# Kernel optimization log

Hardware: AMD Instinct MI355X
Metric: run time of the kernel (lower is better)

Reference implementation:

```python
import jax, jax.numpy as jnp
import numpy as np

B, V, S, D, H, G = 8, 321, 24, 256, 8, 10
K = -(-V // G)   # num_per_group = ceil(var_num/groups) = 33
DFF = 1024
DH = D // H

PARAM_SHAPES = dict(
    queries=(B, V, S, D),
    t_wq=(D, D), t_bq=(D,), t_wk=(D, D), t_bk=(D,), t_wv=(D, D), t_bv=(D,), t_wo=(D, D), t_bo=(D,),
    s_wq=(D, D), s_bq=(D,), s_wk=(D, D), s_bk=(D,), s_wv=(D, D), s_bv=(D,), s_wo=(D, D), s_bo=(D,),
    cluster=(S, G, D), conv_w=(G, K), conv_b=(G,),
    r_wq=(D, D), r_bq=(D,), r_wk=(D, D), r_bk=(D,), r_wv=(D, D), r_bv=(D,), r_wo=(D, D), r_bo=(D,),
    ln_t1_g=(D,), ln_t1_b=(D,), ln_t2_g=(D,), ln_t2_b=(D,),
    ln_d1_g=(D,), ln_d1_b=(D,), ln_d2_g=(D,), ln_d2_b=(D,),
    ft_w1=(D, DFF), ft_b1=(DFF,), ft_w2=(DFF, D), ft_b2=(D,),
    fd_w1=(D, DFF), fd_b1=(DFF,), fd_w2=(DFF, D), fd_b2=(D,),
)


def setup_inputs() -> dict:
    key = jax.random.key(0)
    out = {}
    for i, (n, sh) in enumerate(PARAM_SHAPES.items()):
        k = jax.random.fold_in(key, i)
        if n == 'queries':
            out[n] = jax.random.normal(k, sh, jnp.float32)
        elif n.startswith('ln') and n.endswith('_g'):
            out[n] = jnp.ones(sh, jnp.float32)
        elif '_b' in n:
            out[n] = jnp.zeros(sh, jnp.float32)
        else:
            out[n] = jax.random.normal(k, sh, jnp.float32) * 0.02
    return out


def _ln(x, g, b):
    m = x.mean(-1, keepdims=True)
    v = ((x - m) ** 2).mean(-1, keepdims=True)
    return (x - m) * jax.lax.rsqrt(v + 1e-5) * g + b


def _mha(xq, xkv, wq, bq, wk, bk, wv, bv, wo, bo):
    # FullAttention (no mask, eval -> no dropout)
    Bq, L, _ = xq.shape
    Skv = xkv.shape[1]
    q = (xq @ wq + bq).reshape(Bq, L, H, DH)
    k = (xkv @ wk + bk).reshape(Bq, Skv, H, DH)
    v = (xkv @ wv + bv).reshape(Bq, Skv, H, DH)
    A = jax.nn.softmax(jnp.einsum('blhe,bshe->bhls', q, k) / jnp.sqrt(jnp.float32(DH)), axis=-1)
    o = jnp.einsum('bhls,bshd->blhd', A, v).reshape(Bq, L, D)
    return o @ wo + bo


def _ffn(x, w1, b1, w2, b2):
    return jax.nn.gelu(x @ w1 + b1, approximate=False) @ w2 + b2


def _scx(x, wq, bq, wk, bk, wv, bv, wo, bo, cluster, conv_w, conv_b):
    # SCX_Block: top-k cluster routing + gather + grouped 1x1 conv + min-max/exp
    bs = x.shape[0]  # B*S
    xl = jnp.log(jax.nn.relu(x) + 1.0)
    cl = jnp.tile(cluster, (bs // S, 1, 1))                      # (bs, G, D)
    q = (cl @ wq + bq).reshape(bs, G, H, DH).transpose(0, 2, 1, 3)
    k = (xl @ wk + bk).reshape(bs, V, H, DH).transpose(0, 2, 1, 3)
    v = (xl @ wv + bv).reshape(bs, V, H, DH).transpose(0, 2, 1, 3)
    scores = jnp.einsum('bhge,bhve->bhgv', q, k) / jnp.sqrt(jnp.float32(DH))
    _, idx = jax.lax.top_k(scores, K)                            # (bs, H, G, K)
    gathered = jnp.take_along_axis(v[:, :, None, :, :], idx[..., None], axis=3)  # (bs,H,G,K,DH)
    # grouped Conv1d, kernel_size=1 -> per-group weighted sum over K channels
    mixed = jnp.einsum('bhgkd,gk->bhgd', gathered, conv_w) + conv_b[None, None, :, None]
    xmin = mixed.min(-1, keepdims=True)
    xmax = mixed.max(-1, keepdims=True)
    xn = jnp.exp((mixed - xmin) / jnp.maximum(xmax - xmin, 1e-6))
    feat = xn.transpose(0, 2, 1, 3).reshape(bs, G, D)            # 'bs h g d -> bs g (h d)'
    return feat @ wo + bo


def _forward(queries, t_wq, t_bq, t_wk, t_bk, t_wv, t_bv, t_wo, t_bo, s_wq, s_bq, s_wk, s_bk, s_wv, s_bv, s_wo, s_bo, cluster, conv_w, conv_b, r_wq, r_bq, r_wk, r_bk, r_wv, r_bv, r_wo, r_bo, ln_t1_g, ln_t1_b, ln_t2_g, ln_t2_b, ln_d1_g, ln_d1_b, ln_d2_g, ln_d2_b, ft_w1, ft_b1, ft_w2, ft_b2, fd_w1, fd_b1, fd_w2, fd_b2):
    # Route 1: temporal path over segments within each variable
    x = queries.reshape(B * V, S, D)
    x = x + _mha(x, x, t_wq, t_bq, t_wk, t_bk, t_wv, t_bv, t_wo, t_bo)
    x = _ln(x, ln_t1_g, ln_t1_b)
    x = _ln(x + _ffn(x, ft_w1, ft_b1, ft_w2, ft_b2), ln_t2_g, ln_t2_b)
    # Route 2: dimensional path across variables, per segment
    xd = x.reshape(B, V, S, D).transpose(0, 2, 1, 3).reshape(B * S, V, D)
    route = _scx(xd, s_wq, s_bq, s_wk, s_bk, s_wv, s_bv, s_wo, s_bo, cluster, conv_w, conv_b)
    xd = xd + _mha(xd, route, r_wq, r_bq, r_wk, r_bk, r_wv, r_bv, r_wo, r_bo)
    xd = _ln(xd, ln_d1_g, ln_d1_b)
    xd = _ln(xd + _ffn(xd, fd_w1, fd_b1, fd_w2, fd_b2), ln_d2_g, ln_d2_b)
    return xd.reshape(B, S, V, D).transpose(0, 2, 1, 3)


def reference(queries, t_wq, t_bq, t_wk, t_bk, t_wv, t_bv, t_wo, t_bo, s_wq, s_bq, s_wk, s_bk, s_wv, s_bv, s_wo, s_bo, cluster, conv_w, conv_b, r_wq, r_bq, r_wk, r_bk, r_wv, r_bv, r_wo, r_bo, ln_t1_g, ln_t1_b, ln_t2_g, ln_t2_b, ln_d1_g, ln_d1_b, ln_d2_g, ln_d2_b, ft_w1, ft_b1, ft_w2, ft_b2, fd_w1, fd_b1, fd_w2, fd_b2):
    return _forward(queries, t_wq, t_bq, t_wk, t_bk, t_wv, t_bv, t_wo, t_bo, s_wq, s_bq, s_wk, s_bk, s_wv, s_bv, s_wo, s_bo, cluster, conv_w, conv_b, r_wq, r_bq, r_wk, r_bk, r_wv, r_bv, r_wo, r_bo, ln_t1_g, ln_t1_b, ln_t2_g, ln_t2_b, ln_d1_g, ln_d1_b, ln_d2_g, ln_d2_b, ft_w1, ft_b1, ft_w2, ft_b2, fd_w1, fd_b1, fd_w2, fd_b2)
```

## Files before the change

### kernel.cpp

```cpp
#include <hip/hip_runtime.h>
#include <hip/hip_bf16.h>
#include <cmath>

typedef __hip_bfloat16 bf16;
typedef __attribute__((ext_vector_type(8))) short short8;
typedef __attribute__((ext_vector_type(4))) float f32x4;
typedef unsigned int u32;
typedef __attribute__((address_space(3))) u32 lds_u32;
typedef const __attribute__((address_space(1))) u32 glob_u32;

#define BB 8
#define VV 321
#define SS 24
#define DD 256
#define HH 8
#define GG 10
#define KTOP 33
#define DFFN 1024
#define BV (BB*VV)
#define BSEG (BB*SS)
#define NROWS (BV*SS)
#define NE ((size_t)NROWS*DD)
#define SCALE 0.17677669529663687f
#define A2CH 4

enum { GF_GELU=1, GF_LOGRELU=2, GF_ABF16=4, GF_RBF16=8, GF_CBF16=16 };
enum { MF_GELU=1, MF_RF32=8, MF_CF32=16, MF_SPLIT=32, MF_SWZ=64 };

__device__ __forceinline__ float bf2f(bf16 x){ return __bfloat162float(x); }
__device__ __forceinline__ unsigned short f2bfbits(float f){
  bf16 h = __float2bfloat16(f);
  return *(unsigned short*)&h;
}
__device__ __forceinline__ float bfbits2f(unsigned int u){
  bf16 h; *(unsigned short*)&h = (unsigned short)u; return __bfloat162float(h);
}
__device__ __forceinline__ void ld4bf(const bf16* p, float* f){
  uint2 u = *(const uint2*)p;
  f[0]=bfbits2f(u.x&0xffff); f[1]=bfbits2f(u.x>>16);
  f[2]=bfbits2f(u.y&0xffff); f[3]=bfbits2f(u.y>>16);
}
__device__ __forceinline__ void st4bf(bf16* p, const float* f){
  uint2 u;
  u.x = (unsigned)f2bfbits(f[0]) | ((unsigned)f2bfbits(f[1])<<16);
  u.y = (unsigned)f2bfbits(f[2]) | ((unsigned)f2bfbits(f[3])<<16);
  *(uint2*)p = u;
}
__device__ __forceinline__ void gl_lds16(const void* g, void* l){
  __builtin_amdgcn_global_load_lds((glob_u32*)g, (lds_u32*)l, 16, 0, 0);
}

struct WPrep {
  const float* src[12];
  int K[12], N[12], dstoff[12], tileoff[13];
};

__global__ __launch_bounds__(256) void prep_w_k(WPrep p, bf16* __restrict__ pool)
{
  __shared__ float t[32][33];
  int b = blockIdx.x;
  int m = 0;
  while (b >= p.tileoff[m+1]) ++m;
  int tt = b - p.tileoff[m];
  int K = p.K[m], N = p.N[m];
  int nc = N >> 5;
  int tr = tt / nc, tc = tt % nc;
  const float* src = p.src[m];
  int tid = threadIdx.x;
  int r = tid >> 3, c = (tid & 7) * 4;
  float4 v = *(const float4*)&src[(size_t)(tr*32 + r)*N + tc*32 + c];
  t[r][c+0]=v.x; t[r][c+1]=v.y; t[r][c+2]=v.z; t[r][c+3]=v.w;
  __syncthreads();
  bf16* dst = pool + p.dstoff[m];
  size_t base = (size_t)(tc*32 + r)*K + tr*32 + c;
  #pragma unroll
  for (int i=0;i<4;++i) dst[base+i] = __float2bfloat16(t[c+i][r]);
}

__global__ __launch_bounds__(256) void f2b_k(const float* __restrict__ X, bf16* __restrict__ Y, size_t n)
{
  size_t i = ((size_t)blockIdx.x*256 + threadIdx.x)*8;
  if (i >= n) return;
  float4 a = *(const float4*)(X+i);
  float4 b = *(const float4*)(X+i+4);
  unsigned short v[8] = {f2bfbits(a.x),f2bfbits(a.y),f2bfbits(a.z),f2bfbits(a.w),
                         f2bfbits(b.x),f2bfbits(b.y),f2bfbits(b.z),f2bfbits(b.w)};
  *(uint4*)(Y+i) = *(uint4*)v;
}

__global__ __launch_bounds__(256) void mgemm128_k(
    const bf16* __restrict__ Ap, const bf16* __restrict__ Wt,
    const float* __restrict__ bias0, const float* __restrict__ bias1,
    const float* __restrict__ bias2, const void* __restrict__ Rp,
    void* __restrict__ Cp, int M, int N, int K, int flags, size_t splitStride)
{
  __shared__ __align__(16) unsigned short As[2][128*32];
  __shared__ __align__(16) unsigned short Bs[2][128*32];
  int tid = threadIdx.x;
  int wave = tid >> 6, lane = tid & 63;
  int quad = lane >> 4, l16 = lane & 15;
  int wr = wave >> 1, wc = wave & 1;

  int nwgx = gridDim.x;
  int b    = blockIdx.y * nwgx + blockIdx.x;
  int wgid = b;
  if (flags & MF_SWZ) {
    int nwg = nwgx * gridDim.y;
    int q8 = nwg >> 3, r8 = nwg & 7;
    int xcd = b & 7, slot = b >> 3;
    wgid = (xcd < r8 ? xcd*(q8+1) : r8*(q8+1) + (xcd-r8)*q8) + slot;
  }
  int m0 = (wgid / nwgx) * 128, n0 = (wgid % nwgx) * 128;

  f32x4 acc[4][4];
  #pragma unroll
  for (int i=0;i<4;++i)
    #pragma unroll
    for (int j=0;j<4;++j) acc[i][j] = (f32x4){0.f,0.f,0.f,0.f};

  int r0 = wave*32 + (lane>>2);
  int r1 = r0 + 16;
  int kc = (lane&3)*8;
  int gm0 = m0 + r0; if (gm0 >= M) gm0 = M-1;
  int gm1 = m0 + r1; if (gm1 >= M) gm1 = M-1;
  const bf16* gA0 = Ap + (size_t)gm0*K + kc;
  const bf16* gA1 = Ap + (size_t)gm1*K + kc;
  const bf16* gB0 = Wt + (size_t)(n0 + r0)*K + kc;
  const bf16* gB1 = Wt + (size_t)(n0 + r1)*K + kc;

  gl_lds16(gA0, &As[0][wave*1024]);
  gl_lds16(gA1, &As[0][wave*1024 + 512]);
  gl_lds16(gB0, &Bs[0][wave*1024]);
  gl_lds16(gB1, &Bs[0][wave*1024 + 512]);
  __syncthreads();

  int cur = 0;
  for (int k0 = 0; k0 < K; k0 += 32) {
    if (k0 + 32 < K) {
      int nxt = cur ^ 1;
      gl_lds16(gA0 + k0 + 32, &As[nxt][wave*1024]);
      gl_lds16(gA1 + k0 + 32, &As[nxt][wave*1024 + 512]);
      gl_lds16(gB0 + k0 + 32, &Bs[nxt][wave*1024]);
      gl_lds16(gB1 + k0 + 32, &Bs[nxt][wave*1024 + 512]);
    }
    short8 a[4], bb[4];
    #pragma unroll
    for (int i=0;i<4;++i)
      a[i] = *(const short8*)&As[cur][(wr*64 + i*16 + l16)*32 + quad*8];
    #pragma unroll
    for (int j=0;j<4;++j)
      bb[j] = *(const short8*)&Bs[cur][(wc*64 + j*16 + l16)*32 + quad*8];
    #pragma unroll
    for (int i=0;i<4;++i)
      #pragma unroll
      for (int j=0;j<4;++j)
        acc[i][j] = __builtin_amdgcn_mfma_f32_16x16x32_bf16(a[i], bb[j], acc[i][j], 0, 0, 0);
    __syncthreads();
    cur ^= 1;
  }

  #pragma unroll
  for (int i=0;i<4;++i) {
    int mbase = m0 + wr*64 + i*16 + quad*4;
    #pragma unroll
    for (int j=0;j<4;++j) {
      int n = n0 + wc*64 + j*16 + l16;
      float bv;
      if (flags & MF_SPLIT) {
        int sel = n >> 8;
        const float* bp = (sel==0) ? bias0 : (sel==1 ? bias1 : bias2);
        bv = bp[n & 255];
      } else bv = bias0[n];
      #pragma unroll
      for (int r=0;r<4;++r) {
        int mm = mbase + r;
        if (mm >= M) continue;
        float v = acc[i][j][r] + bv;
        if (flags & MF_GELU) v = 0.5f*v*(1.f + erff(v*0.70710678118654752f));
        if (Rp) {
          size_t ri = (size_t)mm*N + n;
          v += (flags & MF_RF32) ? ((const float*)Rp)[ri] : bf2f(((const bf16*)Rp)[ri]);
        }
        if (flags & MF_SPLIT) {
          size_t ci = (size_t)(n>>8)*splitStride + (size_t)mm*256 + (n & 255);
          ((bf16*)Cp)[ci] = __float2bfloat16(v);
        } else {
          size_t ci = (size_t)mm*N + n;
          if (flags & MF_CF32) ((float*)Cp)[ci] = v;
          else                 ((bf16*)Cp)[ci] = __float2bfloat16(v);
        }
      }
    }
  }
}

__global__ __launch_bounds__(512) void mgemm_k(
    const bf16* __restrict__ Ap, const bf16* __restrict__ Wt,
    const float* __restrict__ bias0, const float* __restrict__ bias1,
    const float* __restrict__ bias2, const void* __restrict__ Rp,
    void* __restrict__ Cp, int M, int N, int K, int flags, size_t splitStride)
{
  __shared__ __align__(16) unsigned short As[2][256*32];
  __shared__ __align__(16) unsigned short Bs[2][128*32];
  int tid = threadIdx.x;
  int wave = tid >> 6, lane = tid & 63;
  int quad = lane >> 4, l16 = lane & 15;
  int wr = wave >> 1, wc = wave & 1;

  int nwgx = gridDim.x;
  int b    = blockIdx.y * nwgx + blockIdx.x;
  int wgid = b;
  if (flags & MF_SWZ) {
    int nwg = nwgx * gridDim.y;
    int q8 = nwg >> 3, r8 = nwg & 7;
    int xcd = b & 7, slot = b >> 3;
    wgid = (xcd < r8 ? xcd*(q8+1) : r8*(q8+1) + (xcd-r8)*q8) + slot;
  }
  int m0 = (wgid / nwgx) * 256, n0 = (wgid % nwgx) * 128;

  f32x4 acc[4][4];
  #pragma unroll
  for (int i=0;i<4;++i)
    #pragma unroll
    for (int j=0;j<4;++j) acc[i][j] = (f32x4){0.f,0.f,0.f,0.f};

  int rA0 = wave*32 + (lane>>2);
  int rA1 = rA0 + 16;
  int rB  = wave*16 + (lane>>2);
  int kc = (lane&3)*8;
  int gm0 = m0 + rA0; if (gm0 >= M) gm0 = M-1;
  int gm1 = m0 + rA1; if (gm1 >= M) gm1 = M-1;
  const bf16* gA0 = Ap + (size_t)gm0*K + kc;
  const bf16* gA1 = Ap + (size_t)gm1*K + kc;
  const bf16* gB  = Wt + (size_t)(n0 + rB)*K + kc;

  gl_lds16(gA0, &As[0][wave*1024]);
  gl_lds16(gA1, &As[0][wave*1024 + 512]);
  gl_lds16(gB,  &Bs[0][wave*512]);
  __syncthreads();

  int cur = 0;
  for (int k0 = 0; k0 < K; k0 += 32) {
    if (k0 + 32 < K) {
      int nxt = cur ^ 1;
      gl_lds16(gA0 + k0 + 32, &As[nxt][wave*1024]);
      gl_lds16(gA1 + k0 + 32, &As[nxt][wave*1024 + 512]);
      gl_lds16(gB  + k0 + 32, &Bs[nxt][wave*512]);
    }
    short8 a[4], bb[4];
    #pragma unroll
    for (int i=0;i<4;++i)
      a[i] = *(const short8*)&As[cur][(wr*64 + i*16 + l16)*32 + quad*8];
    #pragma unroll
    for (int j=0;j<4;++j)
      bb[j] = *(const short8*)&Bs[cur][(wc*64 + j*16 + l16)*32 + quad*8];
    #pragma unroll
    for (int i=0;i<4;++i)
      #pragma unroll
      for (int j=0;j<4;++j)
        acc[i][j] = __builtin_amdgcn_mfma_f32_16x16x32_bf16(a[i], bb[j], acc[i][j], 0, 0, 0);
    __syncthreads();
    cur ^= 1;
  }

  #pragma unroll
  for (int i=0;i<4;++i) {
    int mbase = m0 + wr*64 + i*16 + quad*4;
    #pragma unroll
    for (int j=0;j<4;++j) {
      int n = n0 + wc*64 + j*16 + l16;
      float bv;
      if (flags & MF_SPLIT) {
        int sel = n >> 8;
        const float* bp = (sel==0) ? bias0 : (sel==1 ? bias1 : bias2);
        bv = bp[n & 255];
      } else bv = bias0[n];
      #pragma unroll
      for (int r=0;r<4;++r) {
        int mm = mbase + r;
        if (mm >= M) continue;
        float v = acc[i][j][r] + bv;
        if (flags & MF_GELU) v = 0.5f*v*(1.f + erff(v*0.70710678118654752f));
        if (Rp) {
          size_t ri = (size_t)mm*N + n;
          v += (flags & MF_RF32) ? ((const float*)Rp)[ri] : bf2f(((const bf16*)Rp)[ri]);
        }
        if (flags & MF_SPLIT) {
          size_t ci = (size_t)(n>>8)*splitStride + (size_t)mm*256 + (n & 255);
          ((bf16*)Cp)[ci] = __float2bfloat16(v);
        } else {
          size_t ci = (size_t)mm*N + n;
          if (flags & MF_CF32) ((float*)Cp)[ci] = v;
          else                 ((bf16*)Cp)[ci] = __float2bfloat16(v);
        }
      }
    }
  }
}

__global__ __launch_bounds__(256) void gemm_k(
    const void* __restrict__ Ap, const float* __restrict__ W,
    const float* __restrict__ bias, const void* __restrict__ Rp,
    void* __restrict__ Cp, int M, int N, int K, int flags)
{
  __shared__ float As[16][68];
  __shared__ float Ws[16][68];
  int tid = threadIdx.x;
  int tx = tid & 15, ty = tid >> 4;
  int m0 = blockIdx.y * 64, n0 = blockIdx.x * 64;
  float acc[4][4];
  #pragma unroll
  for (int i=0;i<4;i++)
    #pragma unroll
    for (int j=0;j<4;j++) acc[i][j]=0.f;

  for (int k0 = 0; k0 < K; k0 += 16) {
    #pragma unroll
    for (int i = 0; i < 4; ++i) {
      int idx = tid + i*256;
      int r = idx >> 4, c = idx & 15;
      int gr = m0 + r;
      float v = 0.f;
      if (gr < M) {
        size_t gi = (size_t)gr*K + (size_t)(k0 + c);
        v = (flags & GF_ABF16) ? bf2f(((const bf16*)Ap)[gi]) : ((const float*)Ap)[gi];
        if (flags & GF_LOGRELU) v = log1pf(fmaxf(v, 0.f));
      }
      As[c][r] = v;
    }
    #pragma unroll
    for (int i = 0; i < 4; ++i) {
      int idx = tid + i*256;
      int c = idx >> 6, j = idx & 63;
      Ws[c][j] = W[(size_t)(k0+c)*N + (size_t)(n0 + j)];
    }
    __syncthreads();
    #pragma unroll
    for (int k = 0; k < 16; ++k) {
      float a[4], b[4];
      #pragma unroll
      for (int i=0;i<4;i++) a[i] = As[k][ty*4+i];
      #pragma unroll
      for (int j=0;j<4;j++) b[j] = Ws[k][tx*4+j];
      #pragma unroll
      for (int i=0;i<4;i++)
        #pragma unroll
        for (int j=0;j<4;j++) acc[i][j] = fmaf(a[i], b[j], acc[i][j]);
    }
    __syncthreads();
  }
  #pragma unroll
  for (int i=0;i<4;i++) {
    int row = m0 + ty*4 + i;
    if (row >= M) continue;
    #pragma unroll
    for (int j=0;j<4;j++) {
      int col = n0 + tx*4 + j;
      float v = acc[i][j] + bias[col];
      if (flags & GF_GELU) v = 0.5f*v*(1.f + erff(v*0.70710678118654752f));
      if (Rp) {
        size_t ri = (size_t)row*N + col;
        v += (flags & GF_RBF16) ? bf2f(((const bf16*)Rp)[ri]) : ((const float*)Rp)[ri];
      }
      size_t ci = (size_t)row*N + col;
      if (flags & GF_CBF16) ((bf16*)Cp)[ci] = __float2bfloat16(v);
      else                  ((float*)Cp)[ci] = v;
    }
  }
}

__global__ __launch_bounds__(256) void attn1_k(bf16* __restrict__ Q,
                                               const bf16* __restrict__ Kb,
                                               const bf16* __restrict__ Vb)
{
  __shared__ __align__(16) unsigned short lds[4*4096];
  int wave = threadIdx.x >> 6, lane = threadIdx.x & 63;
  int quad = lane >> 4, l16 = lane & 15;
  int p = blockIdx.x*4 + wave;
  int bv = p >> 3, h = p & 7;
  const size_t base0 = ((size_t)bv*SS)*DD + h*32;

  int slab = wave*4096;
  int lQ = slab, lK = slab + 1024, lV = slab + 2048, lP = slab + 3072;

  {
    int row0 = lane >> 2, c0 = (lane & 3)*8;
    const bf16* gq = Q  + base0 + (size_t)row0*DD + c0;
    const bf16* gk = Kb + base0 + (size_t)row0*DD + c0;
    const bf16* gv = Vb + base0 + (size_t)row0*DD + c0;
    gl_lds16(gq, &lds[lQ]);
    gl_lds16(gk, &lds[lK]);
    gl_lds16(gv, &lds[lV]);
    if (lane < 32) {
      int row1 = 16 + (lane >> 2);
      const bf16* gq1 = Q  + base0 + (size_t)row1*DD + c0;
      const bf16* gk1 = Kb + base0 + (size_t)row1*DD + c0;
      const bf16* gv1 = Vb + base0 + (size_t)row1*DD + c0;
      gl_lds16(gq1, &lds[lQ + 512]);
      gl_lds16(gk1, &lds[lK + 512]);
      gl_lds16(gv1, &lds[lV + 512]);
    }
  }
  *(uint2*)&lds[lV + 768 + lane*4] = (uint2){0u,0u};

  asm volatile("s_waitcnt vmcnt(0)" ::: "memory");
  __builtin_amdgcn_sched_barrier(0);

  short8 qa[2], kb[2];
  #pragma unroll
  for (int t=0;t<2;++t) {
    qa[t] = *(const short8*)&lds[lQ + (t*16 + l16)*32 + quad*8];
    kb[t] = *(const short8*)&lds[lK + (t*16 + l16)*32 + quad*8];
  }
  f32x4 scc[2][2];
  #pragma unroll
  for (int ti=0;ti<2;++ti)
    #pragma unroll
    for (int tj=0;tj<2;++tj)
      scc[ti][tj] = __builtin_amdgcn_mfma_f32_16x16x32_bf16(qa[ti], kb[tj],
                      (f32x4){0.f,0.f,0.f,0.f}, 0, 0, 0);
  if (l16 >= 8) {
    scc[0][1] = (f32x4){-INFINITY,-INFINITY,-INFINITY,-INFINITY};
    scc[1][1] = (f32x4){-INFINITY,-INFINITY,-INFINITY,-INFINITY};
  }

  #pragma unroll
  for (int ti=0;ti<2;++ti) {
    #pragma unroll
    for (int r=0;r<4;++r) {
      float mv = fmaxf(scc[ti][0][r], scc[ti][1][r]);
      #pragma unroll
      for (int off=1; off<16; off<<=1) mv = fmaxf(mv, __shfl_xor(mv, off));
      float e0 = expf((scc[ti][0][r]-mv)*SCALE);
      float e1 = expf((scc[ti][1][r]-mv)*SCALE);
      float sm = e0 + e1;
      #pragma unroll
      for (int off=1; off<16; off<<=1) sm += __shfl_xor(sm, off);
      float inv = 1.f/sm;
      int row = ti*16 + quad*4 + r;
      lds[lP + row*32 + l16]      = f2bfbits(e0*inv);
      lds[lP + row*32 + 16 + l16] = f2bfbits(e1*inv);
    }
  }

  f32x4 o[2][2];
  #pragma unroll
  for (int ti=0;ti<2;++ti) {
    short8 pa = *(const short8*)&lds[lP + (ti*16 + l16)*32 + quad*8];
    #pragma unroll
    for (int tn=0;tn<2;++tn) {
      unsigned short vt[8];
      #pragma unroll
      for (int e=0;e<8;++e) vt[e] = lds[lV + (quad*8+e)*32 + tn*16 + l16];
      short8 vb = *(short8*)vt;
      o[ti][tn] = __builtin_amdgcn_mfma_f32_16x16x32_bf16(pa, vb,
                    (f32x4){0.f,0.f,0.f,0.f}, 0, 0, 0);
    }
  }

  #pragma unroll
  for (int ti=0;ti<2;++ti) {
    #pragma unroll
    for (int r=0;r<4;++r) {
      int row = ti*16 + quad*4 + r;
      if (row < SS) {
        #pragma unroll
        for (int tn=0;tn<2;++tn)
          Q[base0 + (size_t)row*DD + tn*16 + l16] = __float2bfloat16(o[ti][tn][r]);
      }
    }
  }
}

__global__ __launch_bounds__(256) void ln_k(const bf16* __restrict__ X, bf16* __restrict__ Y,
                                            const float* __restrict__ g, const float* __restrict__ b,
                                            int nrows)
{
  int row = blockIdx.x*4 + (threadIdx.x >> 6);
  int lane = threadIdx.x & 63;
  if (row >= nrows) return;
  const bf16* xr = X + (size_t)row*DD;
  int c = lane*4;
  float v[4]; ld4bf(xr + c, v);
  float s = v[0]+v[1]+v[2]+v[3];
  #pragma unroll
  for (int off = 32; off; off >>= 1) s += __shfl_xor(s, off);
  float m = s * (1.f/256.f);
  float d0=v[0]-m, d1=v[1]-m, d2=v[2]-m, d3=v[3]-m;
  float q = d0*d0+d1*d1+d2*d2+d3*d3;
  #pragma unroll
  for (int off = 32; off; off >>= 1) q += __shfl_xor(q, off);
  float rstd = rsqrtf(q*(1.f/256.f) + 1e-5f);
  float4 gv = *(const float4*)(g + c);
  float4 bv = *(const float4*)(b + c);
  float o[4] = {d0*rstd*gv.x + bv.x, d1*rstd*gv.y + bv.y,
                d2*rstd*gv.z + bv.z, d3*rstd*gv.w + bv.w};
  st4bf(Y + (size_t)row*DD + c, o);
}

__global__ __launch_bounds__(256) void ln_t_k(const bf16* __restrict__ X, bf16* __restrict__ Y,
                                              bf16* __restrict__ Yl,
                                              const float* __restrict__ g, const float* __restrict__ b)
{
  int r1 = blockIdx.x*4 + (threadIdx.x >> 6);
  int lane = threadIdx.x & 63;
  if (r1 >= NROWS) return;
  const bf16* xr = X + (size_t)r1*DD;
  int c = lane*4;
  float v[4]; ld4bf(xr + c, v);
  float s = v[0]+v[1]+v[2]+v[3];
  #pragma unroll
  for (int off = 32; off; off >>= 1) s += __shfl_xor(s, off);
  float m = s * (1.f/256.f);
  float d0=v[0]-m, d1=v[1]-m, d2=v[2]-m, d3=v[3]-m;
  float q = d0*d0+d1*d1+d2*d2+d3*d3;
  #pragma unroll
  for (int off = 32; off; off >>= 1) q += __shfl_xor(q, off);
  float rstd = rsqrtf(q*(1.f/256.f) + 1e-5f);
  int b_ = r1 / (VV*SS);
  int rem = r1 % (VV*SS);
  int vv = rem / SS, ss = rem % SS;
  int r2 = (b_*SS + ss)*VV + vv;
  float4 gv = *(const float4*)(g + c);
  float4 bvv = *(const float4*)(b + c);
  float o[4] = {d0*rstd*gv.x + bvv.x, d1*rstd*gv.y + bvv.y,
                d2*rstd*gv.z + bvv.z, d3*rstd*gv.w + bvv.w};
  st4bf(Y + (size_t)r2*DD + c, o);
  float ol[4] = {log1pf(fmaxf(o[0],0.f)), log1pf(fmaxf(o[1],0.f)),
                 log1pf(fmaxf(o[2],0.f)), log1pf(fmaxf(o[3],0.f))};
  st4bf(Yl + (size_t)r2*DD + c, ol);
}

__global__ __launch_bounds__(256) void ln_out_k(const bf16* __restrict__ X, float* __restrict__ out,
                                                const float* __restrict__ g, const float* __restrict__ b)
{
  int row = blockIdx.x*4 + (threadIdx.x >> 6);
  int lane = threadIdx.x & 63;
  if (row >= NROWS) return;
  const bf16* xr = X + (size_t)row*DD;
  int c = lane*4;
  float v[4]; ld4bf(xr + c, v);
  float s = v[0]+v[1]+v[2]+v[3];
  #pragma unroll
  for (int off = 32; off; off >>= 1) s += __shfl_xor(s, off);
  float m = s * (1.f/256.f);
  float d0=v[0]-m, d1=v[1]-m, d2=v[2]-m, d3=v[3]-m;
  float q = d0*d0+d1*d1+d2*d2+d3*d3;
  #pragma unroll
  for (int off = 32; off; off >>= 1) q += __shfl_xor(q, off);
  float rstd = rsqrtf(q*(1.f/256.f) + 1e-5f);
  int bs = row / VV, vv = row % VV;
  int bb = bs / SS, ss = bs % SS;
  float* op = out + (((size_t)bb*VV + vv)*SS + ss)*DD + c;
  float4 gv = *(const float4*)(g + c);
  float4 bv = *(const float4*)(b + c);
  float4 ov = {d0*rstd*gv.x + bv.x, d1*rstd*gv.y + bv.y,
               d2*rstd*gv.z + bv.z, d3*rstd*gv.w + bv.w};
  *(float4*)op = ov;
}

__global__ __launch_bounds__(64) void topk_k(const float* __restrict__ qS,
                                             const bf16* __restrict__ kS,
                                             int* __restrict__ idxOut)
{
  int bid = blockIdx.x;
  int g = bid % GG;
  int h = (bid / GG) % HH;
  int bs = bid / (GG*HH);
  int s = bs % SS;
  int lane = threadIdx.x;

  float qv[32];
  const float4* qp = (const float4*)(qS + ((size_t)(s*GG + g))*DD + h*32);
  #pragma unroll
  for (int e4 = 0; e4 < 8; ++e4) {
    float4 t = qp[e4];
    qv[e4*4+0]=t.x; qv[e4*4+1]=t.y; qv[e4*4+2]=t.z; qv[e4*4+3]=t.w;
  }

  float sc[6];
  #pragma unroll
  for (int j = 0; j < 6; ++j) {
    int v = lane + j*64;
    if (v < VV) {
      const uint4* kp = (const uint4*)(kS + ((size_t)bs*VV + v)*DD + h*32);
      float d = 0.f;
      #pragma unroll
      for (int cch = 0; cch < 4; ++cch) {
        uint4 u = kp[cch];
        const unsigned short* usp = (const unsigned short*)&u;
        #pragma unroll
        for (int e = 0; e < 8; ++e)
          d = fmaf(bfbits2f(usp[e]), qv[cch*8+e], d);
      }
      sc[j] = d * SCALE;
    } else sc[j] = -INFINITY;
  }

  for (int it = 0; it < KTOP; ++it) {
    float bv = sc[0]; int bj = 0;
    #pragma unroll
    for (int j = 1; j < 6; ++j) if (sc[j] > bv) { bv = sc[j]; bj = j; }
    int bi = lane + bj*64;
    #pragma unroll
    for (int off = 32; off; off >>= 1) {
      float ov = __shfl_down(bv, off);
      int   oi = __shfl_down(bi, off);
      if (ov > bv || (ov == bv && oi < bi)) { bv = ov; bi = oi; }
    }
    bi = __shfl(bi, 0);
    if (lane == 0) idxOut[(size_t)bid*KTOP + it] = bi;
    if ((bi & 63) == lane) {
      int jj = bi >> 6;
      #pragma unroll
      for (int j = 0; j < 6; ++j) if (jj == j) sc[j] = -INFINITY;
    }
  }
}

__global__ __launch_bounds__(256) void conv_k(const bf16* __restrict__ vS,
                                              const int* __restrict__ idx,
                                              const float* __restrict__ cw,
                                              const float* __restrict__ cb,
                                              float* __restrict__ feat)
{
  int bid = blockIdx.x;
  int bs = bid / GG, g = bid % GG;
  int tid = threadIdx.x;
  int h = tid >> 5, d = tid & 31;
  __shared__ float cws[KTOP];
  __shared__ int idl[HH][KTOP];
  __shared__ float ms[256];
  if (tid < KTOP) cws[tid] = cw[g*KTOP + tid];
  for (int i = tid; i < HH*KTOP; i += 256) {
    int hh = i / KTOP, k = i % KTOP;
    int ix = idx[(((size_t)bs*HH + hh)*GG + g)*KTOP + k];
    idl[hh][k] = (ix < 0) ? 0 : (ix >= VV ? VV-1 : ix);
  }
  __syncthreads();
  float acc = 0.f;
  #pragma unroll
  for (int k = 0; k < KTOP; ++k)
    acc += bf2f(vS[((size_t)bs*VV + idl[h][k])*DD + h*32 + d]) * cws[k];
  acc += cb[g];
  ms[tid] = acc;
  __syncthreads();
  float mn = acc, mx = acc;
  #pragma unroll
  for (int j = 0; j < 32; ++j) {
    float t = ms[h*32 + j];
    mn = fminf(mn, t); mx = fmaxf(mx, t);
  }
  float xn = expf((acc - mn) / fmaxf(mx - mn, 1e-6f));
  feat[((size_t)bs*GG + g)*DD + h*32 + d] = xn;
}

__global__ __launch_bounds__(256) void attn2_k(bf16* __restrict__ Q,
                                               const float* __restrict__ KR,
                                               const float* __restrict__ VR)
{
  const int TPC = (VV*HH + A2CH - 1) / A2CH;
  int bs = blockIdx.x / A2CH;
  int chunk = blockIdx.x % A2CH;
  int tid = threadIdx.x;
  __shared__ float kr[GG][DD], vr[GG][DD];
  for (int i = tid; i < GG*DD/4; i += 256) {
    int r = i >> 6, c4 = (i & 63)*4;
    *(float4*)&kr[r][c4] = *(const float4*)&KR[((size_t)bs*GG + r)*DD + c4];
    *(float4*)&vr[r][c4] = *(const float4*)&VR[((size_t)bs*GG + r)*DD + c4];
  }
  __syncthreads();
  int tend = min(VV*HH, (chunk+1)*TPC);
  for (int task = chunk*TPC + tid; task < tend; task += 256) {
    int v = task >> 3, h = task & 7;
    bf16* qp = Q + ((size_t)bs*VV + v)*DD + h*32;
    float qr[32];
    {
      const uint4* qp4 = (const uint4*)qp;
      #pragma unroll
      for (int cch = 0; cch < 4; ++cch) {
        uint4 u = qp4[cch];
        const unsigned short* usp = (const unsigned short*)&u;
        #pragma unroll
        for (int e = 0; e < 8; ++e) qr[cch*8+e] = bfbits2f(usp[e]);
      }
    }
    float sv[GG];
    float mx = -INFINITY;
    #pragma unroll
    for (int gi = 0; gi < GG; ++gi) {
      float dsum = 0.f;
      #pragma unroll
      for (int d = 0; d < 32; ++d) dsum += qr[d]*kr[gi][h*32+d];
      sv[gi] = dsum * SCALE;
      mx = fmaxf(mx, sv[gi]);
    }
    float ssum = 0.f;
    #pragma unroll
    for (int gi = 0; gi < GG; ++gi) { sv[gi] = expf(sv[gi]-mx); ssum += sv[gi]; }
    float inv = 1.f/ssum;
    float o[32];
    #pragma unroll
    for (int d = 0; d < 32; ++d) o[d] = 0.f;
    #pragma unroll
    for (int gi = 0; gi < GG; ++gi) {
      float p = sv[gi]*inv;
      #pragma unroll
      for (int d = 0; d < 32; ++d) o[d] += p*vr[gi][h*32+d];
    }
    #pragma unroll
    for (int c4 = 0; c4 < 8; ++c4) st4bf(qp + c4*4, &o[c4*4]);
  }
}

extern "C" void kernel_launch(void* const* d_in, const int* in_sizes, int n_in,
                              void* d_out, int out_size, void* d_ws, size_t ws_size,
                              hipStream_t stream)
{
  const float* queries=(const float*)d_in[0];
  const float* t_wq=(const float*)d_in[1];  const float* t_bq=(const float*)d_in[2];
  const float* t_wk=(const float*)d_in[3];  const float* t_bk=(const float*)d_in[4];
  const float* t_wv=(const float*)d_in[5];  const float* t_bv=(const float*)d_in[6];
  const float* t_wo=(const float*)d_in[7];  const float* t_bo=(const float*)d_in[8];
  const float* s_wq=(const float*)d_in[9];  const float* s_bq=(const float*)d_in[10];
  const float* s_wk=(const float*)d_in[11]; const float* s_bk=(const float*)d_in[12];
  const float* s_wv=(const float*)d_in[13]; const float* s_bv=(const float*)d_in[14];
  const float* s_wo=(const float*)d_in[15]; const float* s_bo=(const float*)d_in[16];
  const float* cluster=(const float*)d_in[17];
  const float* conv_w=(const float*)d_in[18]; const float* conv_b=(const float*)d_in[19];
  const float* r_wq=(const float*)d_in[20]; const float* r_bq=(const float*)d_in[21];
  const float* r_wk=(const float*)d_in[22]; const float* r_bk=(const float*)d_in[23];
  const float* r_wv=(const float*)d_in[24]; const float* r_bv=(const float*)d_in[25];
  const float* r_wo=(const float*)d_in[26]; const float* r_bo=(const float*)d_in[27];
  const float* ln_t1_g=(const float*)d_in[28]; const float* ln_t1_b=(const float*)d_in[29];
  const float* ln_t2_g=(const float*)d_in[30]; const float* ln_t2_b=(const float*)d_in[31];
  const float* ln_d1_g=(const float*)d_in[32]; const float* ln_d1_b=(const float*)d_in[33];
  const float* ln_d2_g=(const float*)d_in[34]; const float* ln_d2_b=(const float*)d_in[35];
  const float* ft_w1=(const float*)d_in[36]; const float* ft_b1=(const float*)d_in[37];
  const float* ft_w2=(const float*)d_in[38]; const float* ft_b2=(const float*)d_in[39];
  const float* fd_w1=(const float*)d_in[40]; const float* fd_b1=(const float*)d_in[41];
  const float* fd_w2=(const float*)d_in[42]; const float* fd_b2=(const float*)d_in[43];

  bf16* Ab = (bf16*)d_ws;
  bf16* Bb = Ab + NE;
  bf16* Cb = Bb + NE;
  bf16* Db = Cb + NE;
  bf16* WP = Db + NE;
  float* QSf   = (float*)(WP + 1572864);
  float* FEATf = QSf + 240*256;
  float* ROUTEf= FEATf + 1920*256;
  float* KRf   = ROUTEf + 1920*256;
  float* VRf   = KRf + 1920*256;
  int*   IDXb  = (int*)(VRf + 1920*256);

  WPrep wp;
  const float* wsrc[12] = {t_wq,t_wk,t_wv,t_wo,s_wk,s_wv,r_wq,r_wo,ft_w1,ft_w2,fd_w1,fd_w2};
  int wK[12] = {256,256,256,256,256,256,256,256,256,1024,256,1024};
  int wN[12] = {256,256,256,256,256,256,256,256,1024,256,1024,256};
  int off = 0, toff = 0;
  for (int i=0;i<12;++i) {
    wp.src[i]=wsrc[i]; wp.K[i]=wK[i]; wp.N[i]=wN[i];
    wp.dstoff[i]=off; wp.tileoff[i]=toff;
    off += wK[i]*wN[i];
    toff += (wK[i]/32)*(wN[i]/32);
  }
  wp.tileoff[12]=toff;
  prep_w_k<<<toff, 256, 0, stream>>>(wp, WP);
  bf16* Wqkv=WP+wp.dstoff[0];
  bf16* Wo=WP+wp.dstoff[3];
  bf16* Wskv=WP+wp.dstoff[4];
  bf16* Wrq=WP+wp.dstoff[6]; bf16* Wro=WP+wp.dstoff[7];
  bf16* Wf1=WP+wp.dstoff[8]; bf16* Wf2=WP+wp.dstoff[9];
  bf16* Wd1=WP+wp.dstoff[10]; bf16* Wd2=WP+wp.dstoff[11];

  dim3 blk(256);
  dim3 blkG(512);
  const int STRIPE2 = NROWS/2;
  dim3 gQKV128(6, (NROWS+127)/128);
  dim3 gKV(4, (NROWS+255)/256);
  dim3 gBig(2, (NROWS+255)/256);
  dim3 gF1(8, (STRIPE2+255)/256);
  dim3 gF2(2, (STRIPE2+255)/256);
  dim3 gQ(4, 4);
  dim3 gSmall(4, 30);
  const int GCVT = (int)(NE/2048);

  f2b_k<<<GCVT, blk, 0, stream>>>(queries, Db, NE);
  mgemm128_k<<<gQKV128, blk, 0, stream>>>(Db, Wqkv, t_bq, t_bk, t_bv, nullptr, Ab,
                                          NROWS, 768, 256, MF_SPLIT, NE);
  attn1_k<<<(BV*HH)/4, blk, 0, stream>>>(Ab, Bb, Cb);
  mgemm_k<<<gBig, blkG, 0, stream>>>(Ab, Wo, t_bo, nullptr, nullptr, queries, Bb,
                                     NROWS, 256, 256, MF_RF32|MF_SWZ, 0);
  ln_k<<<NROWS/4, blk, 0, stream>>>(Bb, Ab, ln_t1_g, ln_t1_b, NROWS);
  for (int st = 0; st < 2; ++st) {
    size_t ro = (size_t)st * STRIPE2 * DD;
    mgemm_k<<<gF1, blkG, 0, stream>>>(Ab + ro, Wf1, ft_b1, nullptr, nullptr, nullptr, Cb,
                                      STRIPE2, 1024, 256, MF_GELU|MF_SWZ, 0);
    mgemm_k<<<gF2, blkG, 0, stream>>>(Cb, Wf2, ft_b2, nullptr, nullptr, Ab + ro, Bb + ro,
                                      STRIPE2, 256, 1024, MF_SWZ, 0);
  }
  ln_t_k<<<NROWS/4, blk, 0, stream>>>(Bb, Ab, Db, ln_t2_g, ln_t2_b);

  mgemm_k<<<gKV, blkG, 0, stream>>>(Db, Wskv, s_bk, s_bv, nullptr, nullptr, Bb,
                                    NROWS, 512, 256, MF_SPLIT|MF_SWZ, NE);
  gemm_k<<<gQ, blk, 0, stream>>>(cluster, s_wq, s_bq, nullptr, QSf, 240, 256, 256, 0);
  topk_k<<<BSEG*HH*GG, 64, 0, stream>>>(QSf, Bb, IDXb);
  conv_k<<<BSEG*GG, blk, 0, stream>>>(Cb, IDXb, conv_w, conv_b, FEATf);
  gemm_k<<<gSmall, blk, 0, stream>>>(FEATf, s_wo, s_bo, nullptr, ROUTEf, 1920, 256, 256, 0);
  gemm_k<<<gSmall, blk, 0, stream>>>(ROUTEf, r_wk, r_bk, nullptr, KRf, 1920, 256, 256, 0);
  gemm_k<<<gSmall, blk, 0, stream>>>(ROUTEf, r_wv, r_bv, nullptr, VRf, 1920, 256, 256, 0);
  mgemm_k<<<gBig, blkG, 0, stream>>>(Ab, Wrq, r_bq, nullptr, nullptr, nullptr, Bb,
                                     NROWS, 256, 256, MF_SWZ, 0);
  attn2_k<<<BSEG*A2CH, blk, 0, stream>>>(Bb, KRf, VRf);
  mgemm_k<<<gBig, blkG, 0, stream>>>(Bb, Wro, r_bo, nullptr, nullptr, Ab, Cb,
                                     NROWS, 256, 256, MF_SWZ, 0);
  ln_k<<<NROWS/4, blk, 0, stream>>>(Cb, Ab, ln_d1_g, ln_d1_b, NROWS);
  for (int st = 0; st < 2; ++st) {
    size_t ro = (size_t)st * STRIPE2 * DD;
    mgemm_k<<<gF1, blkG, 0, stream>>>(Ab + ro, Wd1, fd_b1, nullptr, nullptr, nullptr, Bb,
                                      STRIPE2, 1024, 256, MF_GELU|MF_SWZ, 0);
    mgemm_k<<<gF2, blkG, 0, stream>>>(Bb, Wd2, fd_b2, nullptr, nullptr, Ab + ro, Db + ro,
                                      STRIPE2, 256, 1024, MF_SWZ, 0);
  }
  ln_out_k<<<NROWS/4, blk, 0, stream>>>(Db, (float*)d_out, ln_d2_g, ln_d2_b);
}
```

Before: 1.304 ms.

## Fuse output projection, residual add and LayerNorm into one GEMM kernel

Result: no change. 1.319 ms (+1.1%).

```diff
diff --git a/kernel.cpp b/kernel.cpp
--- a/kernel.cpp
+++ b/kernel.cpp
@@ -293,6 +293,139 @@
           if (flags & MF_CF32) ((float*)Cp)[ci] = v;
           else                 ((bf16*)Cp)[ci] = __float2bfloat16(v);
         }
+      }
+    }
+  }
+}
+
+__global__ __launch_bounds__(512) void mgemmln_k(
+    const bf16* __restrict__ Ap, const bf16* __restrict__ Wt,
+    const float* __restrict__ bias, const void* __restrict__ Rp, int resf32,
+    bf16* __restrict__ Yp, const float* __restrict__ g, const float* __restrict__ b,
+    int M)
+{
+  const int N = 256, K = 256;
+  __shared__ __align__(16) unsigned short As[2][128*32];
+  __shared__ __align__(16) unsigned short Bs[2][256*32];
+  __shared__ float redS[128][4];
+  __shared__ float redQ[128][4];
+  __shared__ float rowM[128], rowR[128];
+  int tid = threadIdx.x;
+  int wave = tid >> 6, lane = tid & 63;
+  int quad = lane >> 4, l16 = lane & 15;
+  int wr = wave >> 2, wc = wave & 3;
+  int m0 = blockIdx.x * 128;
+
+  f32x4 acc[4][4];
+  #pragma unroll
+  for (int i=0;i<4;++i)
+    #pragma unroll
+    for (int j=0;j<4;++j) acc[i][j] = (f32x4){0.f,0.f,0.f,0.f};
+
+  int rA  = wave*16 + (lane>>2);
+  int rB0 = wave*32 + (lane>>2);
+  int rB1 = rB0 + 16;
+  int kc = (lane&3)*8;
+  int gmA = m0 + rA; if (gmA >= M) gmA = M-1;
+  const bf16* gA  = Ap + (size_t)gmA*K + kc;
+  const bf16* gB0 = Wt + (size_t)rB0*K + kc;
+  const bf16* gB1 = Wt + (size_t)rB1*K + kc;
+
+  gl_lds16(gA,  &As[0][wave*512]);
+  gl_lds16(gB0, &Bs[0][wave*1024]);
+  gl_lds16(gB1, &Bs[0][wave*1024 + 512]);
+  __syncthreads();
+
+  int cur = 0;
+  for (int k0 = 0; k0 < K; k0 += 32) {
+    if (k0 + 32 < K) {
+      int nxt = cur ^ 1;
+      gl_lds16(gA  + k0 + 32, &As[nxt][wave*512]);
+      gl_lds16(gB0 + k0 + 32, &Bs[nxt][wave*1024]);
+      gl_lds16(gB1 + k0 + 32, &Bs[nxt][wave*1024 + 512]);
+    }
+    short8 a[4], bb[4];
+    #pragma unroll
+    for (int i=0;i<4;++i)
+      a[i] = *(const short8*)&As[cur][(wr*64 + i*16 + l16)*32 + quad*8];
+    #pragma unroll
+    for (int j=0;j<4;++j)
+      bb[j] = *(const short8*)&Bs[cur][(wc*64 + j*16 + l16)*32 + quad*8];
+    #pragma unroll
+    for (int i=0;i<4;++i)
+      #pragma unroll
+      for (int j=0;j<4;++j)
+        acc[i][j] = __builtin_amdgcn_mfma_f32_16x16x32_bf16(a[i], bb[j], acc[i][j], 0, 0, 0);
+    __syncthreads();
+    cur ^= 1;
+  }
+
+  #pragma unroll
+  for (int i=0;i<4;++i) {
+    int mbase = m0 + wr*64 + i*16 + quad*4;
+    #pragma unroll
+    for (int j=0;j<4;++j) {
+      int n = wc*64 + j*16 + l16;
+      float bv = bias[n];
+      #pragma unroll
+      for (int r=0;r<4;++r) {
+        int mm = mbase + r;
+        int mi = (mm < M) ? mm : (M-1);
+        float v = acc[i][j][r] + bv;
+        if (Rp) {
+          size_t ri = (size_t)mi*N + n;
+          v += resf32 ? ((const float*)Rp)[ri] : bf2f(((const bf16*)Rp)[ri]);
+        }
+        acc[i][j][r] = v;
+      }
+    }
+  }
+  #pragma unroll
+  for (int i=0;i<4;++i) {
+    #pragma unroll
+    for (int r=0;r<4;++r) {
+      float s = acc[i][0][r] + acc[i][1][r] + acc[i][2][r] + acc[i][3][r];
+      #pragma unroll
+      for (int off=1; off<16; off<<=1) s += __shfl_xor(s, off);
+      if (l16 == 0) redS[wr*64 + i*16 + quad*4 + r][wc] = s;
+    }
+  }
+  __syncthreads();
+  if (tid < 128)
+    rowM[tid] = (redS[tid][0]+redS[tid][1]+redS[tid][2]+redS[tid][3]) * (1.f/256.f);
+  __syncthreads();
+  #pragma unroll
+  for (int i=0;i<4;++i) {
+    #pragma unroll
+    for (int r=0;r<4;++r) {
+      int row = wr*64 + i*16 + quad*4 + r;
+      float m = rowM[row];
+      float q = 0.f;
+      #pragma unroll
+      for (int j=0;j<4;++j) { float d = acc[i][j][r] - m; q += d*d; }
+      #pragma unroll
+      for (int off=1; off<16; off<<=1) q += __shfl_xor(q, off);
+      if (l16 == 0) redQ[row][wc] = q;
+    }
+  }
+  __syncthreads();
+  if (tid < 128)
+    rowR[tid] = rsqrtf((redQ[tid][0]+redQ[tid][1]+redQ[tid][2]+redQ[tid][3]) * (1.f/256.f) + 1e-5f);
+  __syncthreads();
+  #pragma unroll
+  for (int i=0;i<4;++i) {
+    int mbase = m0 + wr*64 + i*16 + quad*4;
+    #pragma unroll
+    for (int j=0;j<4;++j) {
+      int n = wc*64 + j*16 + l16;
+      float gv = g[n], bvv = b[n];
+      #pragma unroll
+      for (int r=0;r<4;++r) {
+        int mm = mbase + r;
+        if (mm >= M) continue;
+        int row = wr*64 + i*16 + quad*4 + r;
+        float d = acc[i][j][r] - rowM[row];
+        Yp[(size_t)mm*N + n] = __float2bfloat16(d*rowR[row]*gv + bvv);
       }
     }
   }
@@ -781,6 +914,7 @@
   dim3 gBig(2, (NROWS+255)/256);
   dim3 gF1(8, (STRIPE2+255)/256);
   dim3 gF2(2, (STRIPE2+255)/256);
+  const int gLN = (NROWS+127)/128;
   dim3 gQ(4, 4);
   dim3 gSmall(4, 30);
   const int GCVT = (int)(NE/2048);
@@ -789,9 +923,8 @@
   mgemm128_k<<<gQKV128, blk, 0, stream>>>(Db, Wqkv, t_bq, t_bk, t_bv, nullptr, Ab,
                                           NROWS, 768, 256, MF_SPLIT, NE);
   attn1_k<<<(BV*HH)/4, blk, 0, stream>>>(Ab, Bb, Cb);
-  mgemm_k<<<gBig, blkG, 0, stream>>>(Ab, Wo, t_bo, nullptr, nullptr, queries, Bb,
-                                     NROWS, 256, 256, MF_RF32|MF_SWZ, 0);
-  ln_k<<<NROWS/4, blk, 0, stream>>>(Bb, Ab, ln_t1_g, ln_t1_b, NROWS);
+  mgemmln_k<<<gLN, blkG, 0, stream>>>(Ab, Wo, t_bo, queries, 1, Ab,
+                                      ln_t1_g, ln_t1_b, NROWS);
   for (int st = 0; st < 2; ++st) {
     size_t ro = (size_t)st * STRIPE2 * DD;
     mgemm_k<<<gF1, blkG, 0, stream>>>(Ab + ro, Wf1, ft_b1, nullptr, nullptr, nullptr, Cb,
@@ -812,9 +945,8 @@
   mgemm_k<<<gBig, blkG, 0, stream>>>(Ab, Wrq, r_bq, nullptr, nullptr, nullptr, Bb,
                                      NROWS, 256, 256, MF_SWZ, 0);
   attn2_k<<<BSEG*A2CH, blk, 0, stream>>>(Bb, KRf, VRf);
-  mgemm_k<<<gBig, blkG, 0, stream>>>(Bb, Wro, r_bo, nullptr, nullptr, Ab, Cb,
-                                     NROWS, 256, 256, MF_SWZ, 0);
-  ln_k<<<NROWS/4, blk, 0, stream>>>(Cb, Ab, ln_d1_g, ln_d1_b, NROWS);
+  mgemmln_k<<<gLN, blkG, 0, stream>>>(Bb, Wro, r_bo, Ab, 0, Ab,
+                                      ln_d1_g, ln_d1_b, NROWS);
   for (int st = 0; st < 2; ++st) {
     size_t ro = (size_t)st * STRIPE2 * DD;
     mgemm_k<<<gF1, blkG, 0, stream>>>(Ab + ro, Wd1, fd_b1, nullptr, nullptr, nullptr, Bb,
```
